# Optimization experiments

Measured on AMD Instinct MI355X. Metric: run time of the kernel, lower is better.

The kernel has to match this reference:

```python
import jax, jax.numpy as jnp
import numpy as np

EPS = 1e-6
CLIP_RATIO = 1.0  # input_clip_ratio


def fwht(x):
    """Fast Walsh-Hadamard transform along last dim (N must be a power of 2).
    Unnormalized; caller divides by sqrt(N) (QuaRot OnlineHadamard convention)."""
    m, n = x.shape
    h = 1
    y = x
    while h < n:  # log2(n) fixed iterations, fine under jit
        y = y.reshape(m, n // (2 * h), 2, h)
        a, b = y[:, :, 0, :], y[:, :, 1, :]
        y = jnp.concatenate([a + b, a - b], axis=-1)  # [m, n//(2h), 2h]
        h *= 2
    return y.reshape(m, n)


def setup_inputs() -> dict:
    key = jax.random.key(0)
    k1, k2, k3 = jax.random.split(key, 3)
    M, IN, OUT = 8192, 4096, 4096
    x = jax.random.normal(k1, (M, IN), dtype=jnp.float32)
    weight = jax.random.normal(k2, (OUT, IN), dtype=jnp.float32) * 0.02
    bias = jax.random.normal(k3, (OUT,), dtype=jnp.float32) * 0.01
    return {"x": x, "weight": weight, "bias": bias}


def reference(x, weight, bias):
    # --- offline weight quantization (quantize_from_float) ---
    # per-output-row symmetric int4: scale = max|w| / 7, clamp min 1e-6
    w_scales = jnp.clip(jnp.max(jnp.abs(weight), axis=1, keepdims=True), EPS, None) / 7.0  # [OUT,1]
    qw = jnp.clip(jnp.round(weight / w_scales), -8, 7)  # int4 values kept in fp32 (exact)

    # --- online Hadamard rotation of activations ---
    n = x.shape[-1]
    x2 = fwht(x) * (1.0 / jnp.sqrt(jnp.float32(n)))

    # --- symmetric per-token int4 activation quantization (QuaRot Quantizer) ---
    sx = jnp.clip(jnp.max(jnp.abs(x2), axis=-1, keepdims=True), EPS, None) * (CLIP_RATIO / 7.0)  # [M,1]
    qx = jnp.clip(jnp.round(x2 / sx), -8, 7)

    qy = jnp.einsum('mk,nk->mn', qx, qw)  # [M, OUT]

    # --- sym_dequant: row scale (activation) * column scale (weight) + bias ---
    y = qy * sx * w_scales.T + bias[None, :]
    return y
```

## Files before the change

kernel.cpp:

```cpp
#include <hip/hip_runtime.h>
#include <hip/hip_bf16.h>
#include <cstdint>

#define QEPS 1e-6f

typedef int v4i __attribute__((ext_vector_type(4)));

__device__ __forceinline__ void gl_lds16(const void* g, void* l) {
  __builtin_amdgcn_global_load_lds(
      (const __attribute__((address_space(1))) void*)g,
      (__attribute__((address_space(3))) void*)l, 16, 0, 0);
}

__global__ __launch_bounds__(256) void wquant_kernel(const float* __restrict__ w,
                                                     int8_t* __restrict__ qw,
                                                     float* __restrict__ wscale) {
  const int n = blockIdx.x;
  const int t = threadIdx.x;
  const float4* wrow = (const float4*)(w + (size_t)n * 4096);
  float4 v[4];
  float am = 0.f;
#pragma unroll
  for (int i = 0; i < 4; ++i) {
    v[i] = wrow[i * 256 + t];
    am = fmaxf(am, fmaxf(fmaxf(fabsf(v[i].x), fabsf(v[i].y)),
                         fmaxf(fabsf(v[i].z), fabsf(v[i].w))));
  }
#pragma unroll
  for (int off = 32; off > 0; off >>= 1)
    am = fmaxf(am, __shfl_down(am, off));
  __shared__ float wm[4];
  if ((t & 63) == 0) wm[t >> 6] = am;
  __syncthreads();
  const float rowmax = fmaxf(fmaxf(wm[0], wm[1]), fmaxf(wm[2], wm[3]));
  const float scale = fmaxf(rowmax, QEPS) / 7.0f;
  if (t == 0) wscale[n] = scale;
  char4* qrow = (char4*)(qw + (size_t)n * 4096);
#pragma unroll
  for (int i = 0; i < 4; ++i) {
    char4 q;
    q.x = (signed char)fminf(fmaxf(rintf(v[i].x / scale), -8.f), 7.f);
    q.y = (signed char)fminf(fmaxf(rintf(v[i].y / scale), -8.f), 7.f);
    q.z = (signed char)fminf(fmaxf(rintf(v[i].z / scale), -8.f), 7.f);
    q.w = (signed char)fminf(fmaxf(rintf(v[i].w / scale), -8.f), 7.f);
    qrow[i * 256 + t] = q;
  }
}

__global__ __launch_bounds__(256) void xquant_kernel(const float* __restrict__ x,
                                                     int8_t* __restrict__ qx,
                                                     float* __restrict__ sx) {
  const int m = blockIdx.x * 4 + (threadIdx.x >> 6);
  const int g = threadIdx.x & 63;
  const float4* xrow = (const float4*)(x + (size_t)m * 4096);
  float4 v[16];
#pragma unroll
  for (int j = 0; j < 16; ++j) v[j] = xrow[j * 64 + g];

#pragma unroll
  for (int j = 0; j < 16; ++j) {
    float a0 = v[j].x, b0 = v[j].y, a1 = v[j].z, b1 = v[j].w;
    v[j].x = a0 + b0; v[j].y = a0 - b0;
    v[j].z = a1 + b1; v[j].w = a1 - b1;
  }
#pragma unroll
  for (int j = 0; j < 16; ++j) {
    float a0 = v[j].x, b0 = v[j].z, a1 = v[j].y, b1 = v[j].w;
    v[j].x = a0 + b0; v[j].z = a0 - b0;
    v[j].y = a1 + b1; v[j].w = a1 - b1;
  }
#pragma unroll
  for (int d = 1; d < 64; d <<= 1) {
    const bool low = (g & d) == 0;
#pragma unroll
    for (int j = 0; j < 16; ++j) {
      float px = __shfl_xor(v[j].x, d);
      float py = __shfl_xor(v[j].y, d);
      float pz = __shfl_xor(v[j].z, d);
      float pw = __shfl_xor(v[j].w, d);
      v[j].x = low ? (v[j].x + px) : (px - v[j].x);
      v[j].y = low ? (v[j].y + py) : (py - v[j].y);
      v[j].z = low ? (v[j].z + pz) : (pz - v[j].z);
      v[j].w = low ? (v[j].w + pw) : (pw - v[j].w);
    }
  }
#pragma unroll
  for (int d = 1; d < 16; d <<= 1) {
#pragma unroll
    for (int j = 0; j < 16; ++j) {
      if ((j & d) == 0) {
        float4 a = v[j], b = v[j + d];
        v[j].x = a.x + b.x; v[j].y = a.y + b.y;
        v[j].z = a.z + b.z; v[j].w = a.w + b.w;
        v[j + d].x = a.x - b.x; v[j + d].y = a.y - b.y;
        v[j + d].z = a.z - b.z; v[j + d].w = a.w - b.w;
      }
    }
  }

  float am = 0.f;
#pragma unroll
  for (int j = 0; j < 16; ++j)
    am = fmaxf(am, fmaxf(fmaxf(fabsf(v[j].x), fabsf(v[j].y)),
                         fmaxf(fabsf(v[j].z), fabsf(v[j].w))));
#pragma unroll
  for (int off = 32; off > 0; off >>= 1)
    am = fmaxf(am, __shfl_xor(am, off));

  const float inv64 = 1.0f / 64.0f;
  const float sxv = fmaxf(am * inv64, QEPS) * (1.0f / 7.0f);
  if (g == 0) sx[m] = sxv;

  char4* qrow = (char4*)(qx + (size_t)m * 4096);
#pragma unroll
  for (int j = 0; j < 16; ++j) {
    char4 q;
    q.x = (signed char)fminf(fmaxf(rintf((v[j].x * inv64) / sxv), -8.f), 7.f);
    q.y = (signed char)fminf(fmaxf(rintf((v[j].y * inv64) / sxv), -8.f), 7.f);
    q.z = (signed char)fminf(fmaxf(rintf((v[j].z * inv64) / sxv), -8.f), 7.f);
    q.w = (signed char)fminf(fmaxf(rintf((v[j].w * inv64) / sxv), -8.f), 7.f);
    qrow[j * 64 + g] = q;
  }
}

#define BM 128
#define BN 128
#define BK 64

__global__ __launch_bounds__(256) void gemm_kernel(const int8_t* __restrict__ qx,
                                                   const int8_t* __restrict__ qw,
                                                   const float* __restrict__ sx,
                                                   const float* __restrict__ wscale,
                                                   const float* __restrict__ bias,
                                                   float* __restrict__ out) {
  __shared__ int8_t As[BM * BK] __attribute__((aligned(16)));
  __shared__ int8_t Bs[BN * BK] __attribute__((aligned(16)));
  const int t = threadIdx.x;
  const int m0 = blockIdx.y * BM;
  const int n0 = blockIdx.x * BN;
  const int lane = t & 63;
  const int wave = t >> 6;
  const int wr = wave >> 1;
  const int wc = wave & 1;
  const int lr = lane & 15;
  const int lq = lane >> 4;

  v4i acc[4][4] = {};

  const int flat0 = t * 16;
  const int row0 = flat0 >> 6;
  const int c_src = (t & 3) ^ ((t >> 3) & 3);
  const int goff = row0 * 4096 + c_src * 16;
  const int8_t* gA0 = qx + (size_t)m0 * 4096 + goff;
  const int8_t* gA1 = qx + (size_t)(m0 + 64) * 4096 + goff;
  const int8_t* gB0 = qw + (size_t)n0 * 4096 + goff;
  const int8_t* gB1 = qw + (size_t)(n0 + 64) * 4096 + goff;

  const int swz = (lr >> 1) & 3;
  int aoff[4], boff[4];
#pragma unroll
  for (int i = 0; i < 4; ++i) {
    aoff[i] = (wr * 64 + i * 16 + lr) * 64 + ((lq ^ swz) * 16);
    boff[i] = (wc * 64 + i * 16 + lr) * 64 + ((lq ^ swz) * 16);
  }

  for (int k0 = 0; k0 < 4096; k0 += BK) {
    __syncthreads();
    gl_lds16(gA0 + k0, As + flat0);
    gl_lds16(gA1 + k0, As + 4096 + flat0);
    gl_lds16(gB0 + k0, Bs + flat0);
    gl_lds16(gB1 + k0, Bs + 4096 + flat0);
    __syncthreads();

    v4i a[4], b[4];
#pragma unroll
    for (int mt = 0; mt < 4; ++mt) a[mt] = *(const v4i*)(As + aoff[mt]);
#pragma unroll
    for (int nt = 0; nt < 4; ++nt) b[nt] = *(const v4i*)(Bs + boff[nt]);
#pragma unroll
    for (int mt = 0; mt < 4; ++mt)
#pragma unroll
      for (int nt = 0; nt < 4; ++nt)
        acc[mt][nt] = __builtin_amdgcn_mfma_i32_16x16x64_i8(a[mt], b[nt], acc[mt][nt], 0, 0, 0);
  }

#pragma unroll
  for (int mt = 0; mt < 4; ++mt) {
#pragma unroll
    for (int r = 0; r < 4; ++r) {
      const int m = m0 + wr * 64 + mt * 16 + lq * 4 + r;
      const float sm = sx[m];
#pragma unroll
      for (int nt = 0; nt < 4; ++nt) {
        const int n = n0 + wc * 64 + nt * 16 + lr;
        out[(size_t)m * 4096 + n] = (float)acc[mt][nt][r] * sm * wscale[n] + bias[n];
      }
    }
  }
}

extern "C" void kernel_launch(void* const* d_in, const int* in_sizes, int n_in,
                              void* d_out, int out_size, void* d_ws, size_t ws_size,
                              hipStream_t stream) {
  const float* x = (const float*)d_in[0];
  const float* w = (const float*)d_in[1];
  const float* bias = (const float*)d_in[2];
  float* out = (float*)d_out;

  int8_t* qx = (int8_t*)d_ws;
  int8_t* qw = qx + (size_t)8192 * 4096;
  float* wscale = (float*)(qw + (size_t)4096 * 4096);
  float* sxp = wscale + 4096;

  wquant_kernel<<<4096, 256, 0, stream>>>(w, qw, wscale);
  xquant_kernel<<<2048, 256, 0, stream>>>(x, qx, sxp);
  dim3 grid(4096 / BN, 8192 / BM);
  gemm_kernel<<<grid, 256, 0, stream>>>(qx, qw, sxp, wscale, bias, out);
}
```

Before: 438.6 us.

## Encode int4 values as FP8 e4m3 and use scaled FP8 MFMA with BK=128

Quantized activations and weights, which are integers in [-8,7], are now stored as exact FP8 e4m3 bytes through a small lookup encoder. The GEMM uses the gfx950 scaled f8f6f4 16x16x128 MFMA with unit scales and accumulates in fp32 instead of the i8 16x16x64 MFMA with int32. BK grows to 128 with a matching XOR swizzle for the LDS loads. The aim is higher MFMA throughput per K step with fewer loop iterations, at the cost of more LDS per block and fp32 accumulation, which stays exact for these magnitudes.

```diff
diff --git a/kernel.cpp b/kernel.cpp
--- a/kernel.cpp
+++ b/kernel.cpp
@@ -5,6 +5,8 @@
 #define QEPS 1e-6f
 
 typedef int v4i __attribute__((ext_vector_type(4)));
+typedef int v8i __attribute__((ext_vector_type(8)));
+typedef float v4f __attribute__((ext_vector_type(4)));
 
 __device__ __forceinline__ void gl_lds16(const void* g, void* l) {
   __builtin_amdgcn_global_load_lds(
@@ -12,8 +14,16 @@
       (__attribute__((address_space(3))) void*)l, 16, 0, 0);
 }
 
+__device__ __forceinline__ uint8_t enc_e4m3(float q) {
+  const int idx = (int)q + 8;
+  const unsigned long long lo = 0xB8C0C4C8CACCCED0ull;
+  const unsigned long long hi = 0x4E4C4A4844403800ull;
+  const unsigned long long tbl = (idx < 8) ? lo : hi;
+  return (uint8_t)(tbl >> ((idx & 7) * 8));
+}
+
 __global__ __launch_bounds__(256) void wquant_kernel(const float* __restrict__ w,
-                                                     int8_t* __restrict__ qw,
+                                                     uint8_t* __restrict__ qw,
                                                      float* __restrict__ wscale) {
   const int n = blockIdx.x;
   const int t = threadIdx.x;
@@ -35,20 +45,20 @@
   const float rowmax = fmaxf(fmaxf(wm[0], wm[1]), fmaxf(wm[2], wm[3]));
   const float scale = fmaxf(rowmax, QEPS) / 7.0f;
   if (t == 0) wscale[n] = scale;
-  char4* qrow = (char4*)(qw + (size_t)n * 4096);
+  uchar4* qrow = (uchar4*)(qw + (size_t)n * 4096);
 #pragma unroll
   for (int i = 0; i < 4; ++i) {
-    char4 q;
-    q.x = (signed char)fminf(fmaxf(rintf(v[i].x / scale), -8.f), 7.f);
-    q.y = (signed char)fminf(fmaxf(rintf(v[i].y / scale), -8.f), 7.f);
-    q.z = (signed char)fminf(fmaxf(rintf(v[i].z / scale), -8.f), 7.f);
-    q.w = (signed char)fminf(fmaxf(rintf(v[i].w / scale), -8.f), 7.f);
+    uchar4 q;
+    q.x = enc_e4m3(fminf(fmaxf(rintf(v[i].x / scale), -8.f), 7.f));
+    q.y = enc_e4m3(fminf(fmaxf(rintf(v[i].y / scale), -8.f), 7.f));
+    q.z = enc_e4m3(fminf(fmaxf(rintf(v[i].z / scale), -8.f), 7.f));
+    q.w = enc_e4m3(fminf(fmaxf(rintf(v[i].w / scale), -8.f), 7.f));
     qrow[i * 256 + t] = q;
   }
 }
 
 __global__ __launch_bounds__(256) void xquant_kernel(const float* __restrict__ x,
-                                                     int8_t* __restrict__ qx,
+                                                     uint8_t* __restrict__ qx,
                                                      float* __restrict__ sx) {
   const int m = blockIdx.x * 4 + (threadIdx.x >> 6);
   const int g = threadIdx.x & 63;
@@ -111,30 +121,30 @@
   const float sxv = fmaxf(am * inv64, QEPS) * (1.0f / 7.0f);
   if (g == 0) sx[m] = sxv;
 
-  char4* qrow = (char4*)(qx + (size_t)m * 4096);
+  uchar4* qrow = (uchar4*)(qx + (size_t)m * 4096);
 #pragma unroll
   for (int j = 0; j < 16; ++j) {
-    char4 q;
-    q.x = (signed char)fminf(fmaxf(rintf((v[j].x * inv64) / sxv), -8.f), 7.f);
-    q.y = (signed char)fminf(fmaxf(rintf((v[j].y * inv64) / sxv), -8.f), 7.f);
-    q.z = (signed char)fminf(fmaxf(rintf((v[j].z * inv64) / sxv), -8.f), 7.f);
-    q.w = (signed char)fminf(fmaxf(rintf((v[j].w * inv64) / sxv), -8.f), 7.f);
+    uchar4 q;
+    q.x = enc_e4m3(fminf(fmaxf(rintf((v[j].x * inv64) / sxv), -8.f), 7.f));
+    q.y = enc_e4m3(fminf(fmaxf(rintf((v[j].y * inv64) / sxv), -8.f), 7.f));
+    q.z = enc_e4m3(fminf(fmaxf(rintf((v[j].z * inv64) / sxv), -8.f), 7.f));
+    q.w = enc_e4m3(fminf(fmaxf(rintf((v[j].w * inv64) / sxv), -8.f), 7.f));
     qrow[j * 64 + g] = q;
   }
 }
 
 #define BM 128
 #define BN 128
-#define BK 64
-
-__global__ __launch_bounds__(256) void gemm_kernel(const int8_t* __restrict__ qx,
-                                                   const int8_t* __restrict__ qw,
+#define BK 128
+
+__global__ __launch_bounds__(256) void gemm_kernel(const uint8_t* __restrict__ qx,
+                                                   const uint8_t* __restrict__ qw,
                                                    const float* __restrict__ sx,
                                                    const float* __restrict__ wscale,
                                                    const float* __restrict__ bias,
                                                    float* __restrict__ out) {
-  __shared__ int8_t As[BM * BK] __attribute__((aligned(16)));
-  __shared__ int8_t Bs[BN * BK] __attribute__((aligned(16)));
+  __shared__ uint8_t As[BM * BK] __attribute__((aligned(16)));
+  __shared__ uint8_t Bs[BN * BK] __attribute__((aligned(16)));
   const int t = threadIdx.x;
   const int m0 = blockIdx.y * BM;
   const int n0 = blockIdx.x * BN;
@@ -145,43 +155,53 @@
   const int lr = lane & 15;
   const int lq = lane >> 4;
 
-  v4i acc[4][4] = {};
-
-  const int flat0 = t * 16;
-  const int row0 = flat0 >> 6;
-  const int c_src = (t & 3) ^ ((t >> 3) & 3);
-  const int goff = row0 * 4096 + c_src * 16;
-  const int8_t* gA0 = qx + (size_t)m0 * 4096 + goff;
-  const int8_t* gA1 = qx + (size_t)(m0 + 64) * 4096 + goff;
-  const int8_t* gB0 = qw + (size_t)n0 * 4096 + goff;
-  const int8_t* gB1 = qw + (size_t)(n0 + 64) * 4096 + goff;
-
-  const int swz = (lr >> 1) & 3;
-  int aoff[4], boff[4];
+  v4f acc[4][4] = {};
+
+  const int rA = t >> 3;
+  const int csrc16 = (((t & 7) ^ (rA & 7)) << 4);
+  const uint8_t* ga = qx + (size_t)(m0 + rA) * 4096 + csrc16;
+  const uint8_t* gb = qw + (size_t)(n0 + rA) * 4096 + csrc16;
+  const int ldst = t * 16;
+
+  const int r7 = lr & 7;
+  int aoff0[4], aoff1[4], boff0[4], boff1[4];
 #pragma unroll
   for (int i = 0; i < 4; ++i) {
-    aoff[i] = (wr * 64 + i * 16 + lr) * 64 + ((lq ^ swz) * 16);
-    boff[i] = (wc * 64 + i * 16 + lr) * 64 + ((lq ^ swz) * 16);
+    const int rowa = (wr * 64 + i * 16 + lr) * 128;
+    const int rowb = (wc * 64 + i * 16 + lr) * 128;
+    aoff0[i] = rowa + (((2 * lq) ^ r7) << 4);
+    aoff1[i] = rowa + (((2 * lq + 1) ^ r7) << 4);
+    boff0[i] = rowb + (((2 * lq) ^ r7) << 4);
+    boff1[i] = rowb + (((2 * lq + 1) ^ r7) << 4);
   }
 
   for (int k0 = 0; k0 < 4096; k0 += BK) {
     __syncthreads();
-    gl_lds16(gA0 + k0, As + flat0);
-    gl_lds16(gA1 + k0, As + 4096 + flat0);
-    gl_lds16(gB0 + k0, Bs + flat0);
-    gl_lds16(gB1 + k0, Bs + 4096 + flat0);
+#pragma unroll
+    for (int i = 0; i < 4; ++i) {
+      gl_lds16(ga + k0 + (size_t)i * 32 * 4096, As + i * 4096 + ldst);
+      gl_lds16(gb + k0 + (size_t)i * 32 * 4096, Bs + i * 4096 + ldst);
+    }
     __syncthreads();
 
-    v4i a[4], b[4];
-#pragma unroll
-    for (int mt = 0; mt < 4; ++mt) a[mt] = *(const v4i*)(As + aoff[mt]);
-#pragma unroll
-    for (int nt = 0; nt < 4; ++nt) b[nt] = *(const v4i*)(Bs + boff[nt]);
+    union frag { v8i v; v4i h[2]; };
+    frag a[4], b[4];
+#pragma unroll
+    for (int i = 0; i < 4; ++i) {
+      a[i].h[0] = *(const v4i*)(As + aoff0[i]);
+      a[i].h[1] = *(const v4i*)(As + aoff1[i]);
+      b[i].h[0] = *(const v4i*)(Bs + boff0[i]);
+      b[i].h[1] = *(const v4i*)(Bs + boff1[i]);
+    }
 #pragma unroll
     for (int mt = 0; mt < 4; ++mt)
 #pragma unroll
       for (int nt = 0; nt < 4; ++nt)
-        acc[mt][nt] = __builtin_amdgcn_mfma_i32_16x16x64_i8(a[mt], b[nt], acc[mt][nt], 0, 0, 0);
+        acc[mt][nt] = __builtin_amdgcn_mfma_scale_f32_16x16x128_f8f6f4(
+            a[mt].v, b[nt].v, acc[mt][nt],
+            0, 0,
+            0, 0x7F7F7F7F,
+            0, 0x7F7F7F7F);
   }
 
 #pragma unroll
@@ -193,7 +213,7 @@
 #pragma unroll
       for (int nt = 0; nt < 4; ++nt) {
         const int n = n0 + wc * 64 + nt * 16 + lr;
-        out[(size_t)m * 4096 + n] = (float)acc[mt][nt][r] * sm * wscale[n] + bias[n];
+        out[(size_t)m * 4096 + n] = acc[mt][nt][r] * sm * wscale[n] + bias[n];
       }
     }
   }
@@ -207,8 +227,8 @@
   const float* bias = (const float*)d_in[2];
   float* out = (float*)d_out;
 
-  int8_t* qx = (int8_t*)d_ws;
-  int8_t* qw = qx + (size_t)8192 * 4096;
+  uint8_t* qx = (uint8_t*)d_ws;
+  uint8_t* qw = qx + (size_t)8192 * 4096;
   float* wscale = (float*)(qw + (size_t)4096 * 4096);
   float* sxp = wscale + 4096;
 
```

New measurement: 417.6 us. 1.05x faster.
